# Performance work log

Measured on AMD Instinct MI355X. Metric: run time of the kernel, lower is better.

Reference implementation:

```python
import jax, jax.numpy as jnp
import numpy as np

NEG_SLOPE = 0.2


def setup_inputs() -> dict:
    key = jax.random.key(0)
    k1, k2, k3, k4, k5, k6 = jax.random.split(key, 6)
    N, E, IN, OUT = 100000, 1600000, 256, 32
    feat = jax.random.normal(k1, (N, IN), dtype=jnp.float32)
    W = jax.random.normal(k2, (IN, OUT), dtype=jnp.float32) * (1.0 / np.sqrt(IN))
    attn_l = jax.random.normal(k3, (OUT,), dtype=jnp.float32) * 0.1
    attn_r = jax.random.normal(k4, (OUT,), dtype=jnp.float32) * 0.1
    bias = jnp.zeros((OUT,), dtype=jnp.float32)
    src = jax.random.randint(k5, (E,), 0, N, dtype=jnp.int32)
    dst = jax.random.randint(k6, (E,), 0, N, dtype=jnp.int32)
    return {"feat": feat, "W": W, "attn_l": attn_l, "attn_r": attn_r,
            "bias": bias, "src": src, "dst": dst}


def reference(feat, W, attn_l, attn_r, bias, src, dst):
    N = feat.shape[0]
    # dense projection: [N, in] @ [in, out] -> [N, out]
    h = feat @ W
    el = h @ attn_l  # [N]
    er = h @ attn_r  # [N]
    # per-edge raw score: el[u] + er[v] for edge u->v
    e = el[src] + er[dst]  # [E]
    e = jnp.where(e > 0, e, NEG_SLOPE * e)  # leaky relu
    # edge softmax grouped by destination node (numerically stable)
    m = jax.ops.segment_max(e, dst, num_segments=N)  # [N], -inf for isolated nodes
    m = jax.lax.stop_gradient(m)
    ex = jnp.exp(e - m[dst])  # [E]
    denom = jax.ops.segment_sum(ex, dst, num_segments=N)  # [N]
    alpha = ex / denom[dst]  # [E]
    # weighted aggregation (sparse SpMM): sum_{u->v} alpha_uv * h[u]
    rst = jax.ops.segment_sum(h[src] * alpha[:, None], dst, num_segments=N)  # [N, out]
    return rst + bias
```

## Files before the change

kernel.cpp:

```cpp
#include <hip/hip_runtime.h>
#include <hip/hip_bf16.h>
#include <math.h>

#define NEG_SLOPE 0.2f
#define BUCK_BITS 5
#define BUCK_NODES 32
#define CAP 800
#define SRC_MASK 0x1FFFFFF
#define NBUK_MAX 3200

#define CBITS 8
#define CNODES 256
#define CAPC 4672
#define NC_MAX 400
#define FB1 512

typedef __bf16 bf16x8 __attribute__((ext_vector_type(8)));
typedef __bf16 bf16x4 __attribute__((ext_vector_type(4)));
typedef float  f32x4  __attribute__((ext_vector_type(4)));

__global__ void prep(const float* __restrict__ W, __bf16* __restrict__ Whi,
                     unsigned int* __restrict__ fcur, int NBUK,
                     unsigned int* __restrict__ ccur, int NC) {
    int idx = blockIdx.x * blockDim.x + threadIdx.x;
    if (idx < NBUK) fcur[idx] = 0u;
    if (idx < NC)   ccur[idx] = 0u;
    if (idx >= 8192) return;
    int j = idx & 7, lane = (idx >> 3) & 63, nt = (idx >> 9) & 1, kt = idx >> 10;
    int q = lane >> 4, c = lane & 15;
    int k = kt * 32 + q * 8 + j;
    int n = nt * 16 + c;
    Whi[idx] = (__bf16)W[k * 32 + n];
}

__global__ __launch_bounds__(256) void gemm_h(const float* __restrict__ feat,
                                              const __bf16* __restrict__ Whi,
                                              const float* __restrict__ attn_l,
                                              const float* __restrict__ attn_r,
                                              __bf16* __restrict__ hb,
                                              float* __restrict__ el,
                                              float* __restrict__ er,
                                              int N, int Ntiles) {
    __shared__ bf16x8 sB[1024];
    int tid = threadIdx.x;
    for (int i = tid; i < 1024; i += 256) sB[i] = ((const bf16x8*)Whi)[i];
    __syncthreads();

    int wid  = blockIdx.x * 4 + (tid >> 6);
    int lane = tid & 63;
    if (wid >= Ntiles) return;

    int c = lane & 15, q = lane >> 4;
    int row = wid * 16 + c;
    if (row >= N) row = N - 1;
    const f32x4* A = (const f32x4*)(feat + (size_t)row * 256 + q * 8);

    f32x4 acc0 = {0.f, 0.f, 0.f, 0.f};
    f32x4 acc1 = {0.f, 0.f, 0.f, 0.f};
#pragma unroll
    for (int kt = 0; kt < 8; kt++) {
        f32x4 a0 = __builtin_nontemporal_load(A + kt * 8);
        f32x4 a1 = __builtin_nontemporal_load(A + kt * 8 + 1);
        bf16x8 ah, al;
#pragma unroll
        for (int j = 0; j < 4; j++) {
            __bf16 h0 = (__bf16)a0[j];
            __bf16 h1 = (__bf16)a1[j];
            ah[j]     = h0;
            ah[j + 4] = h1;
            al[j]     = (__bf16)(a0[j] - (float)h0);
            al[j + 4] = (__bf16)(a1[j] - (float)h1);
        }
        bf16x8 bh0 = sB[(kt * 2 + 0) * 64 + lane];
        bf16x8 bh1 = sB[(kt * 2 + 1) * 64 + lane];
        acc0 = __builtin_amdgcn_mfma_f32_16x16x32_bf16(ah, bh0, acc0, 0, 0, 0);
        acc0 = __builtin_amdgcn_mfma_f32_16x16x32_bf16(al, bh0, acc0, 0, 0, 0);
        acc1 = __builtin_amdgcn_mfma_f32_16x16x32_bf16(ah, bh1, acc1, 0, 0, 0);
        acc1 = __builtin_amdgcn_mfma_f32_16x16x32_bf16(al, bh1, acc1, 0, 0, 0);
    }

    float alc  = attn_l[c],      arc  = attn_r[c];
    float alc2 = attn_l[c + 16], arc2 = attn_r[c + 16];
#pragma unroll
    for (int r = 0; r < 4; r++) {
        int m = wid * 16 + q * 4 + r;
        if (m < N) {
            hb[(size_t)m * 32 + c]      = (__bf16)acc0[r];
            hb[(size_t)m * 32 + 16 + c] = (__bf16)acc1[r];
        }
        float pl = acc0[r] * alc + acc1[r] * alc2;
        float pr = acc0[r] * arc + acc1[r] * arc2;
#pragma unroll
        for (int off = 8; off >= 1; off >>= 1) {
            pl += __shfl_xor(pl, off);
            pr += __shfl_xor(pr, off);
        }
        if (c == 0 && m < N) { el[m] = pl; er[m] = pr; }
    }
}

__global__ __launch_bounds__(512) void bin_coarse(const int* __restrict__ src,
                                                  const int* __restrict__ dst,
                                                  unsigned int* __restrict__ ccur,
                                                  uint2* __restrict__ cbin,
                                                  int E, int NC, int batch) {
    __shared__ unsigned int hist[NC_MAX];
    __shared__ unsigned int cbase[NC_MAX];
    int tid = threadIdx.x;
    int b0 = blockIdx.x * batch;
    int b1 = min(b0 + batch, E);
    for (int i = tid; i < NC; i += 512) hist[i] = 0;
    __syncthreads();
    for (int i = b0 + tid; i < b1; i += 512)
        atomicAdd(&hist[((unsigned)dst[i]) >> CBITS], 1u);
    __syncthreads();
    for (int i = tid; i < NC; i += 512) {
        unsigned c = hist[i];
        cbase[i] = c ? atomicAdd(&ccur[i], c) : 0u;
        hist[i] = 0;
    }
    __syncthreads();
    for (int i = b0 + tid; i < b1; i += 512) {
        int d = dst[i];
        int s = src[i];
        unsigned cb = ((unsigned)d) >> CBITS;
        unsigned r = atomicAdd(&hist[cb], 1u);
        unsigned pos = cbase[cb] + r;
        if (pos < CAPC)
            cbin[(size_t)cb * CAPC + pos] = make_uint2((unsigned)s, (unsigned)d);
    }
}

__global__ __launch_bounds__(256) void refine(const unsigned int* __restrict__ ccur,
                                              const uint2* __restrict__ cbin,
                                              unsigned int* __restrict__ fcur,
                                              unsigned int* __restrict__ fbin,
                                              int NC) {
    __shared__ unsigned int hist[8];
    __shared__ unsigned int basec[8];
    int blk = blockIdx.x;
    int cb = blk >> 1, seg = blk & 1;
    if (cb >= NC) return;
    int tid = threadIdx.x;
    int cnt = (int)min(ccur[cb], (unsigned)CAPC);
    int lo = (cnt * seg) >> 1;
    int hi = (cnt * (seg + 1)) >> 1;

    if (tid < 8) hist[tid] = 0;
    __syncthreads();
    const uint2* cp = cbin + (size_t)cb * CAPC;
    for (int i = lo + tid; i < hi; i += 256)
        atomicAdd(&hist[(cp[i].y >> BUCK_BITS) & 7], 1u);
    __syncthreads();
    if (tid < 8) {
        unsigned v = hist[tid];
        basec[tid] = v ? atomicAdd(&fcur[cb * 8 + tid], v) : 0u;
        hist[tid] = 0;
    }
    __syncthreads();
    for (int i = lo + tid; i < hi; i += 256) {
        uint2 r = cp[i];
        int fb = (r.y >> BUCK_BITS) & 7;
        unsigned rank = atomicAdd(&hist[fb], 1u);
        unsigned pos = basec[fb] + rank;
        if (pos < CAP)
            fbin[(size_t)(cb * 8 + fb) * CAP + pos] =
                ((r.y & (BUCK_NODES - 1)) << 25) | r.x;
    }
}

__global__ __launch_bounds__(256) void aggregate(const unsigned int* __restrict__ cursor,
                                                 const unsigned int* __restrict__ binned,
                                                 const float* __restrict__ el,
                                                 const float* __restrict__ er,
                                                 const __bf16* __restrict__ hb,
                                                 const float* __restrict__ bias,
                                                 float* __restrict__ out, int N) {
    __shared__ uint2        rw_s[CAP];
    __shared__ unsigned int hist[BUCK_NODES];
    __shared__ int          off_s[BUCK_NODES + 1];
    __shared__ float        den[BUCK_NODES];
    __shared__ float        er_l[BUCK_NODES];

    int buck = blockIdx.x;
    int base = buck << BUCK_BITS;
    int nn = min(BUCK_NODES, N - base);
    int tid = threadIdx.x;

    int cnt = (int)min(cursor[buck], (unsigned)CAP);
    const unsigned int* eb = binned + (size_t)buck * CAP;

    if (tid < BUCK_NODES) {
        hist[tid] = 0;
        den[tid] = 0.f;
        er_l[tid] = (tid < nn) ? er[base + tid] : 0.f;
    }
    __syncthreads();

    unsigned int rl[4];
    int k = 0;
    for (int i = tid; i < cnt; i += 256) {
        unsigned r = eb[i];
        rl[k++] = r;
        atomicAdd(&hist[r >> 25], 1u);
    }
    __syncthreads();

    if (tid < BUCK_NODES) {
        int v = (int)hist[tid];
        int orig = v;
#pragma unroll
        for (int off = 1; off < BUCK_NODES; off <<= 1) {
            int x = __shfl_up(v, off, 64);
            if (tid >= off) v += x;
        }
        off_s[tid] = v - orig;
        if (tid == BUCK_NODES - 1) off_s[BUCK_NODES] = v;
        hist[tid] = (unsigned)(v - orig);
    }
    __syncthreads();

    k = 0;
    for (int i = tid; i < cnt; i += 256) {
        unsigned r = rl[k++];
        int s = r & SRC_MASK;
        int d = r >> 25;
        float e = el[s] + er_l[d];
        e = (e > 0.f) ? e : NEG_SLOPE * e;
        float w = __expf(e);
        unsigned pos = atomicAdd(&hist[d], 1u);
        rw_s[pos] = make_uint2((unsigned)s, __float_as_uint(w));
        atomicAdd(&den[d], w);
    }
    __syncthreads();

    int lane = tid & 63, wv = tid >> 6;
    int oct = lane >> 3, t = lane & 7;
    f32x4 b4 = *(const f32x4*)&bias[t * 4];
    for (int n = wv; n < nn; n += 4) {
        float sm = den[n];
        int s0 = off_s[n], s1 = off_s[n + 1];
        f32x4 acc = {0.f, 0.f, 0.f, 0.f};
#pragma unroll 2
        for (int j = s0 + oct; j < s1; j += 8) {
            uint2 rw = rw_s[j];
            float w = __uint_as_float(rw.y);
            bf16x4 hv = *(const bf16x4*)&hb[(size_t)rw.x * 32 + t * 4];
            acc[0] += w * (float)hv[0];
            acc[1] += w * (float)hv[1];
            acc[2] += w * (float)hv[2];
            acc[3] += w * (float)hv[3];
        }
#pragma unroll
        for (int off = 8; off <= 32; off <<= 1) {
            acc[0] += __shfl_xor(acc[0], off);
            acc[1] += __shfl_xor(acc[1], off);
            acc[2] += __shfl_xor(acc[2], off);
            acc[3] += __shfl_xor(acc[3], off);
        }
        if (lane < 8) {
            f32x4 o;
            if (sm > 0.f) {
                float inv = 1.f / sm;
                o[0] = acc[0] * inv + b4[0];
                o[1] = acc[1] * inv + b4[1];
                o[2] = acc[2] * inv + b4[2];
                o[3] = acc[3] * inv + b4[3];
            } else {
                o = b4;
            }
            *(f32x4*)&out[(size_t)(base + n) * 32 + t * 4] = o;
        }
    }
}

static inline size_t align256(size_t x) { return (x + 255) & ~(size_t)255; }

extern "C" void kernel_launch(void* const* d_in, const int* in_sizes, int n_in,
                              void* d_out, int out_size, void* d_ws, size_t ws_size,
                              hipStream_t stream) {
    const float* feat   = (const float*)d_in[0];
    const float* W      = (const float*)d_in[1];
    const float* attn_l = (const float*)d_in[2];
    const float* attn_r = (const float*)d_in[3];
    const float* bias   = (const float*)d_in[4];
    const int* src = (const int*)d_in[5];
    const int* dst = (const int*)d_in[6];
    float* out = (float*)d_out;

    const int IN = 256;
    int N = in_sizes[0] / IN;
    int E = in_sizes[5];
    (void)n_in; (void)out_size; (void)ws_size;

    int Ntiles = (N + 15) / 16;
    int NBUK = (N + BUCK_NODES - 1) >> BUCK_BITS;
    int NC   = (N + CNODES - 1) >> CBITS;
    int batch = (E + FB1 - 1) / FB1;

    char* p = (char*)d_ws;
    __bf16* hb     = (__bf16*)p; p += align256((size_t)N * 32 * 2);
    float* el      = (float*)p; p += align256((size_t)N * 4);
    float* er      = (float*)p; p += align256((size_t)N * 4);
    unsigned int* fcur = (unsigned int*)p; p += align256((size_t)NBUK_MAX * 4);
    unsigned int* fbin = (unsigned int*)p; p += align256((size_t)NBUK * CAP * 4);
    unsigned int* ccur = (unsigned int*)p; p += align256((size_t)NC_MAX * 4);
    uint2*        cbin = (uint2*)p;        p += align256((size_t)NC * CAPC * 8);
    __bf16* Whi    = (__bf16*)p; p += align256((size_t)8192 * 2);

    prep<<<33, 256, 0, stream>>>(W, Whi, fcur, NBUK, ccur, NC);
    gemm_h<<<(Ntiles + 3) / 4, 256, 0, stream>>>(feat, Whi, attn_l, attn_r,
                                                 hb, el, er, N, Ntiles);
    bin_coarse<<<FB1, 512, 0, stream>>>(src, dst, ccur, cbin, E, NC, batch);
    refine<<<NC * 2, 256, 0, stream>>>(ccur, cbin, fcur, fbin, NC);
    aggregate<<<NBUK, 256, 0, stream>>>(fcur, fbin, el, er, hb, bias, out, N);
}
```

Before: 249.6 us.

## Replace two-pass coarse/refine edge binning with direct global-atomic bucketing

```diff
diff --git a/kernel.cpp b/kernel.cpp
--- a/kernel.cpp
+++ b/kernel.cpp
@@ -9,22 +9,14 @@
 #define SRC_MASK 0x1FFFFFF
 #define NBUK_MAX 3200
 
-#define CBITS 8
-#define CNODES 256
-#define CAPC 4672
-#define NC_MAX 400
-#define FB1 512
-
 typedef __bf16 bf16x8 __attribute__((ext_vector_type(8)));
 typedef __bf16 bf16x4 __attribute__((ext_vector_type(4)));
 typedef float  f32x4  __attribute__((ext_vector_type(4)));
 
 __global__ void prep(const float* __restrict__ W, __bf16* __restrict__ Whi,
-                     unsigned int* __restrict__ fcur, int NBUK,
-                     unsigned int* __restrict__ ccur, int NC) {
+                     unsigned int* __restrict__ fcur, int NBUK) {
     int idx = blockIdx.x * blockDim.x + threadIdx.x;
     if (idx < NBUK) fcur[idx] = 0u;
-    if (idx < NC)   ccur[idx] = 0u;
     if (idx >= 8192) return;
     int j = idx & 7, lane = (idx >> 3) & 63, nt = (idx >> 9) & 1, kt = idx >> 10;
     int q = lane >> 4, c = lane & 15;
@@ -99,73 +91,24 @@
     }
 }
 
-__global__ __launch_bounds__(512) void bin_coarse(const int* __restrict__ src,
+__global__ __launch_bounds__(256) void bin_direct(const int* __restrict__ src,
                                                   const int* __restrict__ dst,
-                                                  unsigned int* __restrict__ ccur,
-                                                  uint2* __restrict__ cbin,
-                                                  int E, int NC, int batch) {
-    __shared__ unsigned int hist[NC_MAX];
-    __shared__ unsigned int cbase[NC_MAX];
-    int tid = threadIdx.x;
-    int b0 = blockIdx.x * batch;
-    int b1 = min(b0 + batch, E);
-    for (int i = tid; i < NC; i += 512) hist[i] = 0;
-    __syncthreads();
-    for (int i = b0 + tid; i < b1; i += 512)
-        atomicAdd(&hist[((unsigned)dst[i]) >> CBITS], 1u);
-    __syncthreads();
-    for (int i = tid; i < NC; i += 512) {
-        unsigned c = hist[i];
-        cbase[i] = c ? atomicAdd(&ccur[i], c) : 0u;
-        hist[i] = 0;
-    }
-    __syncthreads();
-    for (int i = b0 + tid; i < b1; i += 512) {
-        int d = dst[i];
-        int s = src[i];
-        unsigned cb = ((unsigned)d) >> CBITS;
-        unsigned r = atomicAdd(&hist[cb], 1u);
-        unsigned pos = cbase[cb] + r;
-        if (pos < CAPC)
-            cbin[(size_t)cb * CAPC + pos] = make_uint2((unsigned)s, (unsigned)d);
-    }
-}
-
-__global__ __launch_bounds__(256) void refine(const unsigned int* __restrict__ ccur,
-                                              const uint2* __restrict__ cbin,
-                                              unsigned int* __restrict__ fcur,
-                                              unsigned int* __restrict__ fbin,
-                                              int NC) {
-    __shared__ unsigned int hist[8];
-    __shared__ unsigned int basec[8];
-    int blk = blockIdx.x;
-    int cb = blk >> 1, seg = blk & 1;
-    if (cb >= NC) return;
-    int tid = threadIdx.x;
-    int cnt = (int)min(ccur[cb], (unsigned)CAPC);
-    int lo = (cnt * seg) >> 1;
-    int hi = (cnt * (seg + 1)) >> 1;
-
-    if (tid < 8) hist[tid] = 0;
-    __syncthreads();
-    const uint2* cp = cbin + (size_t)cb * CAPC;
-    for (int i = lo + tid; i < hi; i += 256)
-        atomicAdd(&hist[(cp[i].y >> BUCK_BITS) & 7], 1u);
-    __syncthreads();
-    if (tid < 8) {
-        unsigned v = hist[tid];
-        basec[tid] = v ? atomicAdd(&fcur[cb * 8 + tid], v) : 0u;
-        hist[tid] = 0;
-    }
-    __syncthreads();
-    for (int i = lo + tid; i < hi; i += 256) {
-        uint2 r = cp[i];
-        int fb = (r.y >> BUCK_BITS) & 7;
-        unsigned rank = atomicAdd(&hist[fb], 1u);
-        unsigned pos = basec[fb] + rank;
+                                                  unsigned int* __restrict__ fcur,
+                                                  unsigned int* __restrict__ fbin,
+                                                  int E4) {
+    int i = blockIdx.x * 256 + threadIdx.x;
+    if (i >= E4) return;
+    int4 ss = ((const int4*)src)[i];
+    int4 dd = ((const int4*)dst)[i];
+#pragma unroll
+    for (int j = 0; j < 4; j++) {
+        int s = (&ss.x)[j];
+        int d = (&dd.x)[j];
+        unsigned fb = ((unsigned)d) >> BUCK_BITS;
+        unsigned pos = atomicAdd(&fcur[fb], 1u);
         if (pos < CAP)
-            fbin[(size_t)(cb * 8 + fb) * CAP + pos] =
-                ((r.y & (BUCK_NODES - 1)) << 25) | r.x;
+            fbin[(size_t)fb * CAP + pos] =
+                ((unsigned)(d & (BUCK_NODES - 1)) << 25) | (unsigned)s;
     }
 }
 
@@ -295,8 +238,7 @@
 
     int Ntiles = (N + 15) / 16;
     int NBUK = (N + BUCK_NODES - 1) >> BUCK_BITS;
-    int NC   = (N + CNODES - 1) >> CBITS;
-    int batch = (E + FB1 - 1) / FB1;
+    int E4 = E >> 2;
 
     char* p = (char*)d_ws;
     __bf16* hb     = (__bf16*)p; p += align256((size_t)N * 32 * 2);
@@ -304,14 +246,11 @@
     float* er      = (float*)p; p += align256((size_t)N * 4);
     unsigned int* fcur = (unsigned int*)p; p += align256((size_t)NBUK_MAX * 4);
     unsigned int* fbin = (unsigned int*)p; p += align256((size_t)NBUK * CAP * 4);
-    unsigned int* ccur = (unsigned int*)p; p += align256((size_t)NC_MAX * 4);
-    uint2*        cbin = (uint2*)p;        p += align256((size_t)NC * CAPC * 8);
     __bf16* Whi    = (__bf16*)p; p += align256((size_t)8192 * 2);
 
-    prep<<<33, 256, 0, stream>>>(W, Whi, fcur, NBUK, ccur, NC);
+    prep<<<33, 256, 0, stream>>>(W, Whi, fcur, NBUK);
     gemm_h<<<(Ntiles + 3) / 4, 256, 0, stream>>>(feat, Whi, attn_l, attn_r,
                                                  hb, el, er, N, Ntiles);
-    bin_coarse<<<FB1, 512, 0, stream>>>(src, dst, ccur, cbin, E, NC, batch);
-    refine<<<NC * 2, 256, 0, stream>>>(ccur, cbin, fcur, fbin, NC);
+    bin_direct<<<(E4 + 255) / 256, 256, 0, stream>>>(src, dst, fcur, fbin, E4);
     aggregate<<<NBUK, 256, 0, stream>>>(fcur, fbin, el, er, hb, bias, out, N);
 }
```

Result: slower. 347.6 us (+39.3%).

## Fuse coarse edge binning into GEMM kernel and pack coarse bin entries

Applied to the files above, without the earlier changes.

```diff
diff --git a/kernel.cpp b/kernel.cpp
--- a/kernel.cpp
+++ b/kernel.cpp
@@ -13,40 +13,82 @@
 #define CNODES 256
 #define CAPC 4672
 #define NC_MAX 400
-#define FB1 512
+#define NBIN 256
 
 typedef __bf16 bf16x8 __attribute__((ext_vector_type(8)));
 typedef __bf16 bf16x4 __attribute__((ext_vector_type(4)));
 typedef float  f32x4  __attribute__((ext_vector_type(4)));
 
-__global__ void prep(const float* __restrict__ W, __bf16* __restrict__ Whi,
-                     unsigned int* __restrict__ fcur, int NBUK,
-                     unsigned int* __restrict__ ccur, int NC) {
+__global__ void zero_cursors(unsigned int* __restrict__ fcur,
+                             unsigned int* __restrict__ ccur) {
     int idx = blockIdx.x * blockDim.x + threadIdx.x;
-    if (idx < NBUK) fcur[idx] = 0u;
-    if (idx < NC)   ccur[idx] = 0u;
-    if (idx >= 8192) return;
-    int j = idx & 7, lane = (idx >> 3) & 63, nt = (idx >> 9) & 1, kt = idx >> 10;
-    int q = lane >> 4, c = lane & 15;
-    int k = kt * 32 + q * 8 + j;
-    int n = nt * 16 + c;
-    Whi[idx] = (__bf16)W[k * 32 + n];
-}
-
-__global__ __launch_bounds__(256) void gemm_h(const float* __restrict__ feat,
-                                              const __bf16* __restrict__ Whi,
-                                              const float* __restrict__ attn_l,
-                                              const float* __restrict__ attn_r,
-                                              __bf16* __restrict__ hb,
-                                              float* __restrict__ el,
-                                              float* __restrict__ er,
-                                              int N, int Ntiles) {
+    if (idx < NBUK_MAX) fcur[idx] = 0u;
+    if (idx < NC_MAX)   ccur[idx] = 0u;
+}
+
+__global__ __launch_bounds__(256) void gemm_bin(const float* __restrict__ feat,
+                                                const float* __restrict__ W,
+                                                const float* __restrict__ attn_l,
+                                                const float* __restrict__ attn_r,
+                                                const int* __restrict__ src,
+                                                const int* __restrict__ dst,
+                                                __bf16* __restrict__ hb,
+                                                float* __restrict__ el,
+                                                float* __restrict__ er,
+                                                unsigned int* __restrict__ ccur,
+                                                unsigned int* __restrict__ cbin,
+                                                int N, int Ntiles, int E, int NC) {
     __shared__ bf16x8 sB[1024];
+    int bid = blockIdx.x;
     int tid = threadIdx.x;
-    for (int i = tid; i < 1024; i += 256) sB[i] = ((const bf16x8*)Whi)[i];
-    __syncthreads();
-
-    int wid  = blockIdx.x * 4 + (tid >> 6);
+    int role, gid;
+    if (bid < 2 * NBIN) { role = bid & 1; gid = bid >> 1; }
+    else                { role = 0;       gid = bid - NBIN; }
+
+    if (role == 1) {
+        unsigned int* hist  = (unsigned int*)sB;
+        unsigned int* cbase = hist + NC_MAX;
+        int batch = (E + NBIN - 1) / NBIN;
+        int b0 = gid * batch;
+        int b1 = min(b0 + batch, E);
+        for (int i = tid; i < NC; i += 256) hist[i] = 0;
+        __syncthreads();
+        for (int i = b0 + tid; i < b1; i += 256)
+            atomicAdd(&hist[((unsigned)dst[i]) >> CBITS], 1u);
+        __syncthreads();
+        for (int i = tid; i < NC; i += 256) {
+            unsigned c = hist[i];
+            cbase[i] = c ? atomicAdd(&ccur[i], c) : 0u;
+            hist[i] = 0;
+        }
+        __syncthreads();
+        for (int i = b0 + tid; i < b1; i += 256) {
+            int d = dst[i];
+            int s = src[i];
+            unsigned cb = ((unsigned)d) >> CBITS;
+            unsigned r = atomicAdd(&hist[cb], 1u);
+            unsigned pos = cbase[cb] + r;
+            if (pos < CAPC)
+                cbin[(size_t)cb * CAPC + pos] =
+                    ((unsigned)(d & (CNODES - 1)) << 17) | (unsigned)s;
+        }
+        return;
+    }
+
+#pragma unroll
+    for (int t = 0; t < 4; t++) {
+        int i = tid + t * 256;
+        int kt = i >> 7, nt = (i >> 6) & 1, ln = i & 63;
+        int qq = ln >> 4, cc = ln & 15;
+        bf16x8 v;
+#pragma unroll
+        for (int j = 0; j < 8; j++)
+            v[j] = (__bf16)W[(kt * 32 + qq * 8 + j) * 32 + nt * 16 + cc];
+        sB[i] = v;
+    }
+    __syncthreads();
+
+    int wid  = gid * 4 + (tid >> 6);
     int lane = tid & 63;
     if (wid >= Ntiles) return;
 
@@ -99,40 +141,8 @@
     }
 }
 
-__global__ __launch_bounds__(512) void bin_coarse(const int* __restrict__ src,
-                                                  const int* __restrict__ dst,
-                                                  unsigned int* __restrict__ ccur,
-                                                  uint2* __restrict__ cbin,
-                                                  int E, int NC, int batch) {
-    __shared__ unsigned int hist[NC_MAX];
-    __shared__ unsigned int cbase[NC_MAX];
-    int tid = threadIdx.x;
-    int b0 = blockIdx.x * batch;
-    int b1 = min(b0 + batch, E);
-    for (int i = tid; i < NC; i += 512) hist[i] = 0;
-    __syncthreads();
-    for (int i = b0 + tid; i < b1; i += 512)
-        atomicAdd(&hist[((unsigned)dst[i]) >> CBITS], 1u);
-    __syncthreads();
-    for (int i = tid; i < NC; i += 512) {
-        unsigned c = hist[i];
-        cbase[i] = c ? atomicAdd(&ccur[i], c) : 0u;
-        hist[i] = 0;
-    }
-    __syncthreads();
-    for (int i = b0 + tid; i < b1; i += 512) {
-        int d = dst[i];
-        int s = src[i];
-        unsigned cb = ((unsigned)d) >> CBITS;
-        unsigned r = atomicAdd(&hist[cb], 1u);
-        unsigned pos = cbase[cb] + r;
-        if (pos < CAPC)
-            cbin[(size_t)cb * CAPC + pos] = make_uint2((unsigned)s, (unsigned)d);
-    }
-}
-
 __global__ __launch_bounds__(256) void refine(const unsigned int* __restrict__ ccur,
-                                              const uint2* __restrict__ cbin,
+                                              const unsigned int* __restrict__ cbin,
                                               unsigned int* __restrict__ fcur,
                                               unsigned int* __restrict__ fbin,
                                               int NC) {
@@ -148,9 +158,14 @@
 
     if (tid < 8) hist[tid] = 0;
     __syncthreads();
-    const uint2* cp = cbin + (size_t)cb * CAPC;
-    for (int i = lo + tid; i < hi; i += 256)
-        atomicAdd(&hist[(cp[i].y >> BUCK_BITS) & 7], 1u);
+    const unsigned int* cp = cbin + (size_t)cb * CAPC;
+    unsigned int rl[10];
+    int k = 0;
+    for (int i = lo + tid; i < hi; i += 256) {
+        unsigned r = cp[i];
+        rl[k++] = r;
+        atomicAdd(&hist[(r >> (17 + BUCK_BITS)) & 7], 1u);
+    }
     __syncthreads();
     if (tid < 8) {
         unsigned v = hist[tid];
@@ -158,14 +173,15 @@
         hist[tid] = 0;
     }
     __syncthreads();
+    k = 0;
     for (int i = lo + tid; i < hi; i += 256) {
-        uint2 r = cp[i];
-        int fb = (r.y >> BUCK_BITS) & 7;
+        unsigned r = rl[k++];
+        int fb = (r >> (17 + BUCK_BITS)) & 7;
         unsigned rank = atomicAdd(&hist[fb], 1u);
         unsigned pos = basec[fb] + rank;
         if (pos < CAP)
             fbin[(size_t)(cb * 8 + fb) * CAP + pos] =
-                ((r.y & (BUCK_NODES - 1)) << 25) | r.x;
+                (((r >> 17) & (BUCK_NODES - 1)) << 25) | (r & 0x1FFFFu);
     }
 }
 
@@ -296,22 +312,21 @@
     int Ntiles = (N + 15) / 16;
     int NBUK = (N + BUCK_NODES - 1) >> BUCK_BITS;
     int NC   = (N + CNODES - 1) >> CBITS;
-    int batch = (E + FB1 - 1) / FB1;
+    int NG   = (Ntiles + 3) / 4;
 
     char* p = (char*)d_ws;
     __bf16* hb     = (__bf16*)p; p += align256((size_t)N * 32 * 2);
     float* el      = (float*)p; p += align256((size_t)N * 4);
     float* er      = (float*)p; p += align256((size_t)N * 4);
     unsigned int* fcur = (unsigned int*)p; p += align256((size_t)NBUK_MAX * 4);
+    unsigned int* ccur = (unsigned int*)p; p += align256((size_t)NC_MAX * 4);
     unsigned int* fbin = (unsigned int*)p; p += align256((size_t)NBUK * CAP * 4);
-    unsigned int* ccur = (unsigned int*)p; p += align256((size_t)NC_MAX * 4);
-    uint2*        cbin = (uint2*)p;        p += align256((size_t)NC * CAPC * 8);
-    __bf16* Whi    = (__bf16*)p; p += align256((size_t)8192 * 2);
-
-    prep<<<33, 256, 0, stream>>>(W, Whi, fcur, NBUK, ccur, NC);
-    gemm_h<<<(Ntiles + 3) / 4, 256, 0, stream>>>(feat, Whi, attn_l, attn_r,
-                                                 hb, el, er, N, Ntiles);
-    bin_coarse<<<FB1, 512, 0, stream>>>(src, dst, ccur, cbin, E, NC, batch);
+    unsigned int* cbin = (unsigned int*)p; p += align256((size_t)NC * CAPC * 4);
+
+    zero_cursors<<<(NBUK_MAX + 255) / 256, 256, 0, stream>>>(fcur, ccur);
+    gemm_bin<<<NG + NBIN, 256, 0, stream>>>(feat, W, attn_l, attn_r, src, dst,
+                                            hb, el, er, ccur, cbin,
+                                            N, Ntiles, E, NC);
     refine<<<NC * 2, 256, 0, stream>>>(ccur, cbin, fcur, fbin, NC);
     aggregate<<<NBUK, 256, 0, stream>>>(fcur, fbin, el, er, hb, bias, out, N);
 }
```

Result: no change. 248.0 us (-0.6%).
